# Kernel optimization log

Hardware: AMD Instinct MI355X
Metric: run time of the kernel (lower is better)

Reference implementation:

```python
import jax, jax.numpy as jnp
import numpy as np

WINDOW_SIZE = 3
STRIDE = 3
CHANNEL = 3
SIGMA = 1.5
C1 = 0.01 ** 2
C2 = 0.03 ** 2


def _make_window():
    # 1D gaussian (sigma=1.5), normalized, outer product -> 2D window, tiled per channel [C,1,ws,ws]
    ws = WINDOW_SIZE
    g = np.exp(-((np.arange(ws) - ws // 2) ** 2) / (2.0 * SIGMA ** 2))
    g = (g / g.sum()).astype(np.float32)
    w2 = np.outer(g, g)
    return jnp.asarray(np.tile(w2[None, None], (CHANNEL, 1, 1, 1)))


def _dwconv(x, w):
    # depthwise conv2d, padding=(ws-1)//2, stride=STRIDE, groups=CHANNEL
    pad = (WINDOW_SIZE - 1) // 2
    return jax.lax.conv_general_dilated(
        x, w,
        window_strides=(STRIDE, STRIDE),
        padding=[(pad, pad), (pad, pad)],
        dimension_numbers=("NCHW", "OIHW", "NCHW"),
        feature_group_count=CHANNEL,
    )


def setup_inputs() -> dict:
    key = jax.random.key(0)
    k1, k2 = jax.random.split(key)
    img1 = jax.random.uniform(k1, (16, 3, 512, 512), dtype=jnp.float32)
    img2 = jax.random.uniform(k2, (16, 3, 512, 512), dtype=jnp.float32)
    return {"img1": img1, "img2": img2, "window": _make_window()}


def reference(img1, img2, window):
    mu1 = _dwconv(img1, window)
    mu2 = _dwconv(img2, window)
    mu1_sq = mu1 * mu1
    mu2_sq = mu2 * mu2
    mu1_mu2 = mu1 * mu2
    sigma1_sq = _dwconv(img1 * img1, window) - mu1_sq
    sigma2_sq = _dwconv(img2 * img2, window) - mu2_sq
    sigma12 = _dwconv(img1 * img2, window) - mu1_mu2
    ssim_map = (2.0 * mu1_mu2 + C1) * (2.0 * sigma12 + C2) / (
        (mu1_sq + mu2_sq + C1) * (sigma1_sq + sigma2_sq + C2)
    )
    # size_average=True -> scalar mean
    return ssim_map.mean()
```

## Files before the change

### kernel.cpp

```cpp
#include <hip/hip_runtime.h>


#define HW       512
#define PLANE_SZ (HW * HW)
#define OHW      171
#define NPLANE   48
#define NOUT     (NPLANE * OHW * OHW)
#define OX4      43
#define NGROUPS  (NPLANE * OHW * OX4)
#define TPB      256
#define NBLK     ((NGROUPS + TPB - 1) / TPB)

typedef float f4 __attribute__((ext_vector_type(4)));

__global__ __launch_bounds__(TPB) void ssim_main(
    const float* __restrict__ img1, const float* __restrict__ img2,
    const float* __restrict__ win, float* __restrict__ partial) {
  float w[9];
#pragma unroll
  for (int i = 0; i < 9; ++i) w[i] = win[i];

  const float C1 = 0.01f * 0.01f;
  const float C2 = 0.03f * 0.03f;

  float acc = 0.0f;
  const int idx = blockIdx.x * TPB + threadIdx.x;
  if (idx < NGROUPS) {
    int ox4 = idx % OX4;
    int t   = idx / OX4;
    int oy  = t % OHW;
    int p   = t / OHW;
    const float* a = img1 + (size_t)p * PLANE_SZ;
    const float* b = img2 + (size_t)p * PLANE_SZ;
    const int iy0 = 3 * oy - 1;
    const int q0  = 3 * ox4 - 1;

    float s1[4]  = {0.f, 0.f, 0.f, 0.f};
    float s2[4]  = {0.f, 0.f, 0.f, 0.f};
    float s11[4] = {0.f, 0.f, 0.f, 0.f};
    float s22[4] = {0.f, 0.f, 0.f, 0.f};
    float s12[4] = {0.f, 0.f, 0.f, 0.f};

#pragma unroll
    for (int r = 0; r < 3; ++r) {
      const int iy = iy0 + r;
      float xa[16], xb[16];
      if (iy >= 0) {
        const f4* pa = (const f4*)(a + (size_t)iy * HW);
        const f4* pb = (const f4*)(b + (size_t)iy * HW);
#pragma unroll
        for (int tq = 0; tq < 4; ++tq) {
          const int q = q0 + tq;
          f4 va = {0.f, 0.f, 0.f, 0.f};
          f4 vb = {0.f, 0.f, 0.f, 0.f};
          if (q >= 0 && q < HW / 4) { va = pa[q]; vb = pb[q]; }
#pragma unroll
          for (int e = 0; e < 4; ++e) { xa[4 * tq + e] = va[e]; xb[4 * tq + e] = vb[e]; }
        }
      } else {
#pragma unroll
        for (int e = 0; e < 16; ++e) { xa[e] = 0.f; xb[e] = 0.f; }
      }
#pragma unroll
      for (int j = 0; j < 4; ++j) {
#pragma unroll
        for (int kx = 0; kx < 3; ++kx) {
          const float wv = w[3 * r + kx];
          const float x = xa[3 * j + 3 + kx];
          const float y = xb[3 * j + 3 + kx];
          s1[j]  += wv * x;
          s2[j]  += wv * y;
          s11[j] += wv * x * x;
          s22[j] += wv * y * y;
          s12[j] += wv * x * y;
        }
      }
    }

    const int oxb = 4 * ox4;
#pragma unroll
    for (int j = 0; j < 4; ++j) {
      if (oxb + j < OHW) {
        const float mu11 = s1[j] * s1[j];
        const float mu22 = s2[j] * s2[j];
        const float mu12 = s1[j] * s2[j];
        const float sg1  = s11[j] - mu11;
        const float sg2  = s22[j] - mu22;
        const float sg12 = s12[j] - mu12;
        const float num = (2.0f * mu12 + C1) * (2.0f * sg12 + C2);
        const float den = (mu11 + mu22 + C1) * (sg1 + sg2 + C2);
        acc += num / den;
      }
    }
  }

#pragma unroll
  for (int off = 32; off > 0; off >>= 1) acc += __shfl_down(acc, off, 64);
  __shared__ float wsum[TPB / 64];
  const int lane = threadIdx.x & 63, wid = threadIdx.x >> 6;
  if (lane == 0) wsum[wid] = acc;
  __syncthreads();
  if (threadIdx.x == 0) {
    float s = 0.f;
#pragma unroll
    for (int i = 0; i < TPB / 64; ++i) s += wsum[i];
    partial[blockIdx.x] = s;
  }
}

__global__ __launch_bounds__(256) void ssim_final(
    const float* __restrict__ partial, float* __restrict__ out) {
  double acc = 0.0;
  for (int i = threadIdx.x; i < NBLK; i += 256) acc += (double)partial[i];
#pragma unroll
  for (int off = 32; off > 0; off >>= 1) acc += __shfl_down(acc, off, 64);
  __shared__ double wsum[4];
  const int lane = threadIdx.x & 63, wid = threadIdx.x >> 6;
  if (lane == 0) wsum[wid] = acc;
  __syncthreads();
  if (threadIdx.x == 0) {
    double s = 0.0;
#pragma unroll
    for (int i = 0; i < 4; ++i) s += wsum[i];
    out[0] = (float)(s / (double)NOUT);
  }
}

extern "C" void kernel_launch(void* const* d_in, const int* in_sizes, int n_in,
                              void* d_out, int out_size, void* d_ws, size_t ws_size,
                              hipStream_t stream) {
  const float* img1 = (const float*)d_in[0];
  const float* img2 = (const float*)d_in[1];
  const float* win  = (const float*)d_in[2];
  float* partial = (float*)d_ws;
  float* out = (float*)d_out;

  ssim_main<<<NBLK, TPB, 0, stream>>>(img1, img2, win, partial);
  ssim_final<<<1, 256, 0, stream>>>(partial, out);
}
```

Before: 132.8 us.

## Assign one wavefront per output row with separable window and lane shuffles

Each wavefront now handles one output row of one plane. Every lane loads two coalesced float4 chunks from each of the three input rows, so each input element is read once instead of through overlapping per-thread windows. The 3x3 window is split into row and column sums, which assumes the window is separable (rank one). Output windows that straddle a lane boundary are completed by passing partial sums between lanes with shuffles. This removes redundant loads and multiply work, at the cost of more complex index arithmetic and shuffle traffic.

```diff
diff --git a/kernel.cpp b/kernel.cpp
--- a/kernel.cpp
+++ b/kernel.cpp
@@ -6,99 +6,133 @@
 #define OHW      171
 #define NPLANE   48
 #define NOUT     (NPLANE * OHW * OHW)
-#define OX4      43
-#define NGROUPS  (NPLANE * OHW * OX4)
+#define NTASK    (NPLANE * OHW)
 #define TPB      256
-#define NBLK     ((NGROUPS + TPB - 1) / TPB)
+#define WPB      4
+#define NBLK     (NTASK / WPB)
 
 typedef float f4 __attribute__((ext_vector_type(4)));
+
+__device__ __forceinline__ float ssim_val(float s1, float s2, float s11,
+                                          float s22, float s12) {
+  const float C1 = 1e-4f, C2 = 9e-4f;
+  const float m11 = s1 * s1, m22 = s2 * s2, m12 = s1 * s2;
+  const float sg1 = s11 - m11, sg2 = s22 - m22, sg12 = s12 - m12;
+  return ((2.0f * m12 + C1) * (2.0f * sg12 + C2)) /
+         ((m11 + m22 + C1) * (sg1 + sg2 + C2));
+}
 
 __global__ __launch_bounds__(TPB) void ssim_main(
     const float* __restrict__ img1, const float* __restrict__ img2,
     const float* __restrict__ win, float* __restrict__ partial) {
-  float w[9];
+  const int lane  = threadIdx.x & 63;
+  const int wv    = threadIdx.x >> 6;
+  const int task  = blockIdx.x * WPB + wv;
+  const int plane = task / OHW;
+  const int oy    = task - plane * OHW;
+
+  float wy[3], wx[3];
 #pragma unroll
-  for (int i = 0; i < 9; ++i) w[i] = win[i];
+  for (int k = 0; k < 3; ++k) {
+    wy[k] = win[3 * k] + win[3 * k + 1] + win[3 * k + 2];
+    wx[k] = win[k] + win[k + 3] + win[k + 6];
+  }
+  const int r0 = 3 * oy - 1;
+  float wyv[3];
+  wyv[0] = (r0 >= 0) ? wy[0] : 0.0f;
+  wyv[1] = wy[1];
+  wyv[2] = wy[2];
+  const int rr0 = (r0 < 0) ? 0 : r0;
 
-  const float C1 = 0.01f * 0.01f;
-  const float C2 = 0.03f * 0.03f;
+  const float* a = img1 + (size_t)plane * PLANE_SZ;
+  const float* b = img2 + (size_t)plane * PLANE_SZ;
+
+  f4 xa[3][2], xb[3][2];
+#pragma unroll
+  for (int k = 0; k < 3; ++k) {
+    const int r = (k == 0) ? rr0 : (r0 + k);
+    const f4* ra = (const f4*)(a + (size_t)r * HW);
+    const f4* rb = (const f4*)(b + (size_t)r * HW);
+    xa[k][0] = ra[lane];      xa[k][1] = ra[lane + 64];
+    xb[k][0] = rb[lane];      xb[k][1] = rb[lane + 64];
+  }
 
   float acc = 0.0f;
-  const int idx = blockIdx.x * TPB + threadIdx.x;
-  if (idx < NGROUPS) {
-    int ox4 = idx % OX4;
-    int t   = idx / OX4;
-    int oy  = t % OHW;
-    int p   = t / OHW;
-    const float* a = img1 + (size_t)p * PLANE_SZ;
-    const float* b = img2 + (size_t)p * PLANE_SZ;
-    const int iy0 = 3 * oy - 1;
-    const int q0  = 3 * ox4 - 1;
-
-    float s1[4]  = {0.f, 0.f, 0.f, 0.f};
-    float s2[4]  = {0.f, 0.f, 0.f, 0.f};
-    float s11[4] = {0.f, 0.f, 0.f, 0.f};
-    float s22[4] = {0.f, 0.f, 0.f, 0.f};
-    float s12[4] = {0.f, 0.f, 0.f, 0.f};
+  float fwd[5];
 
 #pragma unroll
-    for (int r = 0; r < 3; ++r) {
-      const int iy = iy0 + r;
-      float xa[16], xb[16];
-      if (iy >= 0) {
-        const f4* pa = (const f4*)(a + (size_t)iy * HW);
-        const f4* pb = (const f4*)(b + (size_t)iy * HW);
+  for (int c = 0; c < 2; ++c) {
+    const int m = (lane + c) % 3;
+
+    float P1[4]  = {0.f, 0.f, 0.f, 0.f};
+    float P2[4]  = {0.f, 0.f, 0.f, 0.f};
+    float P11[4] = {0.f, 0.f, 0.f, 0.f};
+    float P22[4] = {0.f, 0.f, 0.f, 0.f};
+    float P12[4] = {0.f, 0.f, 0.f, 0.f};
 #pragma unroll
-        for (int tq = 0; tq < 4; ++tq) {
-          const int q = q0 + tq;
-          f4 va = {0.f, 0.f, 0.f, 0.f};
-          f4 vb = {0.f, 0.f, 0.f, 0.f};
-          if (q >= 0 && q < HW / 4) { va = pa[q]; vb = pb[q]; }
-#pragma unroll
-          for (int e = 0; e < 4; ++e) { xa[4 * tq + e] = va[e]; xb[4 * tq + e] = vb[e]; }
-        }
-      } else {
-#pragma unroll
-        for (int e = 0; e < 16; ++e) { xa[e] = 0.f; xb[e] = 0.f; }
-      }
+    for (int k = 0; k < 3; ++k) {
+      const float wyk = wyv[k];
 #pragma unroll
       for (int j = 0; j < 4; ++j) {
-#pragma unroll
-        for (int kx = 0; kx < 3; ++kx) {
-          const float wv = w[3 * r + kx];
-          const float x = xa[3 * j + 3 + kx];
-          const float y = xb[3 * j + 3 + kx];
-          s1[j]  += wv * x;
-          s2[j]  += wv * y;
-          s11[j] += wv * x * x;
-          s22[j] += wv * y * y;
-          s12[j] += wv * x * y;
-        }
+        const float x = xa[k][c][j];
+        const float y = xb[k][c][j];
+        const float u = wyk * x;
+        const float v = wyk * y;
+        P1[j] += u;
+        P2[j] += v;
+        P11[j] = fmaf(u, x, P11[j]);
+        P22[j] = fmaf(v, y, P22[j]);
+        P12[j] = fmaf(u, y, P12[j]);
       }
     }
 
-    const int oxb = 4 * ox4;
+    float wxl[4];
 #pragma unroll
     for (int j = 0; j < 4; ++j) {
-      if (oxb + j < OHW) {
-        const float mu11 = s1[j] * s1[j];
-        const float mu22 = s2[j] * s2[j];
-        const float mu12 = s1[j] * s2[j];
-        const float sg1  = s11[j] - mu11;
-        const float sg2  = s22[j] - mu22;
-        const float sg12 = s12[j] - mu12;
-        const float num = (2.0f * mu12 + C1) * (2.0f * sg12 + C2);
-        const float den = (mu11 + mu22 + C1) * (sg1 + sg2 + C2);
-        acc += num / den;
+      const int ix = (m + j + 1) % 3;
+      wxl[j] = (ix == 0) ? wx[0] : ((ix == 1) ? wx[1] : wx[2]);
+    }
+
+    const float aL = (m != 1) ? 1.0f : 0.0f;
+    const float bL = (m == 2) ? 1.0f : 0.0f;
+    float L[5], R[5];
+    {
+      float t0, t1, t2, t3, full, left;
+#define BIN(Q, P)                                              \
+      t0 = wxl[0] * P[0]; t1 = wxl[1] * P[1];                  \
+      t2 = wxl[2] * P[2]; t3 = wxl[3] * P[3];                  \
+      full = (t0 + t1) + (t2 + t3);                            \
+      left = fmaf(bL, t2, fmaf(aL, t1, t0));                   \
+      L[Q] = left; R[Q] = full - left;
+      BIN(0, P1) BIN(1, P2) BIN(2, P11) BIN(3, P22) BIN(4, P12)
+#undef BIN
+    }
+    if (c == 0) {
+#pragma unroll
+      for (int q = 0; q < 5; ++q) fwd[q] = R[q];
+    }
+
+    const float allow =
+        (m != 2 && !(c == 0 && lane == 0)) ? 1.0f : 0.0f;
+#pragma unroll
+    for (int q = 0; q < 5; ++q) {
+      float up = __shfl_up(R[q], 1, 64);
+      if (c == 1) {
+        const float seam = __shfl(fwd[q], 63, 64);
+        up = (lane == 0) ? seam : up;
       }
+      L[q] = fmaf(allow, up, L[q]);
     }
+
+    const float mR = (m == 1) ? 1.0f : 0.0f;
+    acc += ssim_val(L[0], L[1], L[2], L[3], L[4]);
+    acc += mR * ssim_val(R[0], R[1], R[2], R[3], R[4]);
   }
 
 #pragma unroll
   for (int off = 32; off > 0; off >>= 1) acc += __shfl_down(acc, off, 64);
   __shared__ float wsum[TPB / 64];
-  const int lane = threadIdx.x & 63, wid = threadIdx.x >> 6;
-  if (lane == 0) wsum[wid] = acc;
+  if (lane == 0) wsum[wv] = acc;
   __syncthreads();
   if (threadIdx.x == 0) {
     float s = 0.f;
```

Measured after the change: 119.9 us. -9.7%, faster.
